# Performance work log

Measured on AMD Instinct MI355X. Metric: run time of the kernel, lower is better.

The kernel has to match this reference:

```python
import jax, jax.numpy as jnp
import numpy as np

N = 50000    # num genes (nodes)
E = 500000   # edges per edge type
T = 2        # edge types
L = 2        # gnn layers
H = 4        # attention heads
D = 64       # per-head channels (hidden // heads)
HID = 256    # hidden channels
PRE_IN = 1024
OUT = 64
EPS = 1e-5
SLOPE = 0.2  # PyG GATv2 leaky_relu negative slope


def _layer_norm(x, g, b):
    mu = x.mean(-1, keepdims=True)
    v = x.var(-1, keepdims=True)
    return (x - mu) / jnp.sqrt(v + EPS) * g + b


def _seg_softmax(score, seg, n):
    m = jax.ops.segment_max(score, seg, num_segments=n)
    ex = jnp.exp(score - m[seg])
    den = jax.ops.segment_sum(ex, seg, num_segments=n)
    return ex / (den[seg] + 1e-16)


def _gatv2_projected(x, src, dst, Wl, Wr, att, bias, Wp, bp):
    # GATv2Conv (share_weights=False, concat heads) followed by Linear projection
    n = x.shape[0]
    xl = (x @ Wl).reshape(n, H, D)
    xr = (x @ Wr).reshape(n, H, D)
    hs = xl[src]                                   # [E,H,D] messages from source
    e = jax.nn.leaky_relu(hs + xr[dst], SLOPE)     # [E,H,D]
    score = jnp.einsum('ehd,hd->eh', e, att)       # [E,H]
    alpha = _seg_softmax(score, dst, n)            # softmax over in-edges of dst
    out = jax.ops.segment_sum(hs * alpha[:, :, None], dst, num_segments=n)
    out = out.reshape(n, H * D) + bias             # concat heads + conv bias
    return out @ Wp + bp                           # ProjectedGATConv linear


def setup_inputs() -> dict:
    key = jax.random.key(0)
    ks = jax.random.split(key, 20)
    s = 0.05
    return {
        'x': jax.random.normal(ks[0], (N, PRE_IN), dtype=jnp.float32),
        'edge_index_0': jax.random.randint(ks[1], (2, E), 0, N, dtype=jnp.int32),
        'edge_index_1': jax.random.randint(ks[2], (2, E), 0, N, dtype=jnp.int32),
        'pre_W0': jax.random.normal(ks[3], (PRE_IN, HID)) * s,
        'pre_b0': jnp.zeros((HID,)),
        'pre_g0': jnp.ones((HID,)),
        'pre_be0': jnp.zeros((HID,)),
        'pre_W1': jax.random.normal(ks[4], (HID, HID)) * s,
        'pre_b1': jnp.zeros((HID,)),
        'pre_g1': jnp.ones((HID,)),
        'pre_be1': jnp.zeros((HID,)),
        # HeteroGnn: L layers x T edge types of ProjectedGATConv(GATv2)
        'gat_Wl': jax.random.normal(ks[5], (L, T, HID, H * D)) * s,
        'gat_Wr': jax.random.normal(ks[6], (L, T, HID, H * D)) * s,
        'gat_att': jax.random.normal(ks[7], (L, T, H, D)) * 0.1,
        'gat_bias': jnp.zeros((L, T, H * D)),
        'proj_W': jax.random.normal(ks[8], (L, T, H * D, HID)) * s,
        'proj_b': jnp.zeros((L, T, HID)),
        # prediction head: Linear(HID,HID) + relu + Linear(HID,OUT)
        'head_W0': jax.random.normal(ks[9], (HID, HID)) * s,
        'head_b0': jnp.zeros((HID,)),
        'head_W1': jax.random.normal(ks[10], (HID, OUT)) * s,
        'head_b1': jnp.zeros((OUT,)),
    }


def reference(x, edge_index_0, edge_index_1, pre_W0, pre_b0, pre_g0, pre_be0,
              pre_W1, pre_b1, pre_g1, pre_be1, gat_Wl, gat_Wr, gat_att,
              gat_bias, proj_W, proj_b, head_W0, head_b0, head_W1, head_b1):
    loop = jnp.arange(N, dtype=edge_index_0.dtype)  # add_self_loops=True
    edges = [(jnp.concatenate([ei[0], loop]), jnp.concatenate([ei[1], loop]))
             for ei in (edge_index_0, edge_index_1)]
    # preprocessor MLP
    h = jax.nn.relu(_layer_norm(x @ pre_W0 + pre_b0, pre_g0, pre_be0))
    h = jax.nn.relu(_layer_norm(h @ pre_W1 + pre_b1, pre_g1, pre_be1))
    # hetero GAT stack, HeteroConv aggr='sum'
    for l in range(L):
        acc = jnp.zeros((N, HID), dtype=h.dtype)
        for t in range(T):
            src, dst = edges[t]
            acc = acc + _gatv2_projected(h, src, dst, gat_Wl[l, t], gat_Wr[l, t],
                                         gat_att[l, t], gat_bias[l, t],
                                         proj_W[l, t], proj_b[l, t])
        h = jax.nn.relu(acc)
    # prediction head
    h2 = jax.nn.relu(h @ head_W0 + head_b0)
    return h2 @ head_W1 + head_b1
```

## Files before the change

kernel.cpp:

```cpp
#include <hip/hip_runtime.h>
#include <hip/hip_bf16.h>
#include <math.h>

#define N_NODES 50000
#define MP      50048
#define E_EDGES 500000
#define EPRIME  (E_EDGES + N_NODES)
#define HID     256
#define PRE_IN  1024
#define OUT_DIM 64
#define NHEAD   4
#define DHEAD   64
#define LAYERS  2
#define NTYPES  2

#define SCAN_NBLK 49
#define NPAD      (SCAN_NBLK * 1024)

typedef __attribute__((ext_vector_type(8))) short short8v;
typedef __attribute__((ext_vector_type(4))) float f32x4;
typedef _Float16 h2v __attribute__((ext_vector_type(2)));
typedef _Float16 h8v __attribute__((ext_vector_type(8)));

__device__ __forceinline__ ushort f2bf(float f) {
  uint u = __float_as_uint(f);
  u += 0x7FFF + ((u >> 16) & 1);
  return (ushort)(u >> 16);
}
__device__ __forceinline__ float bf2f(ushort u) {
  return __uint_as_float(((uint)u) << 16);
}

template<bool AF32>
__global__ __launch_bounds__(256) void gemm_k(
    const void* __restrict__ Ap,
    const ushort* __restrict__ Bt,
    int K, int M, int N,
    float*  __restrict__ Cf,
    ushort* __restrict__ Cb,
    const float* __restrict__ bias,
    const float* __restrict__ bias2,
    int do_relu, int out_f16)
{
  __shared__ ushort As[128 * 32];
  __shared__ ushort Bs[64 * 32];
  const int tid = threadIdx.x;
  const int l   = tid & 63;
  const int w   = tid >> 6;
  const int wm  = w & 1;
  const int wn  = w >> 1;
  const int bm  = blockIdx.y * 128;
  const int bn  = blockIdx.x * 64;

  f32x4 acc[4][2];
#pragma unroll
  for (int m = 0; m < 4; m++)
#pragma unroll
    for (int n = 0; n < 2; n++) acc[m][n] = (f32x4){0.f, 0.f, 0.f, 0.f};

  const int srow  = l >> 2;
  const int sslot = l & 3;

  const int brow  = tid >> 2;
  const int bslot = tid & 3;
  const int bkc   = bslot ^ ((brow >> 1) & 3);

  for (int k0 = 0; k0 < K; k0 += 32) {
    {
      const ushort* gb = Bt + (size_t)(bn + brow) * K + k0 + bkc * 8;
      __builtin_amdgcn_global_load_lds(
          (const __attribute__((address_space(1))) uint*)gb,
          (__attribute__((address_space(3))) uint*)((char*)Bs + tid * 16), 16, 0, 0);
    }
#pragma unroll
    for (int i = 0; i < 2; i++) {
      const int row = w * 32 + i * 16 + srow;
      const int kc  = sslot ^ ((row >> 1) & 3);
      const uint off = (uint)row * 64 + (uint)sslot * 16;
      if constexpr (AF32) {
        const float* ga = (const float*)Ap + (size_t)(bm + row) * K + k0 + kc * 8;
        float4 v0 = make_float4(0.f, 0.f, 0.f, 0.f);
        float4 v1 = make_float4(0.f, 0.f, 0.f, 0.f);
        if (bm + row < M) {
          v0 = *reinterpret_cast<const float4*>(ga);
          v1 = *reinterpret_cast<const float4*>(ga + 4);
        }
        short8v s;
        s[0] = (short)f2bf(v0.x); s[1] = (short)f2bf(v0.y);
        s[2] = (short)f2bf(v0.z); s[3] = (short)f2bf(v0.w);
        s[4] = (short)f2bf(v1.x); s[5] = (short)f2bf(v1.y);
        s[6] = (short)f2bf(v1.z); s[7] = (short)f2bf(v1.w);
        *reinterpret_cast<short8v*>((char*)As + off) = s;
      } else {
        const ushort* ga = (const ushort*)Ap + (size_t)(bm + row) * K + k0 + kc * 8;
        __builtin_amdgcn_global_load_lds(
            (const __attribute__((address_space(1))) uint*)ga,
            (__attribute__((address_space(3))) uint*)((char*)As + off), 16, 0, 0);
      }
    }
    __syncthreads();

    short8v a[4], b[2];
#pragma unroll
    for (int m = 0; m < 4; m++) {
      const int row = wm * 64 + m * 16 + (l & 15);
      const int kc  = (l >> 4) ^ ((row >> 1) & 3);
      a[m] = *(const short8v*)((const char*)As + row * 64 + kc * 16);
    }
#pragma unroll
    for (int n = 0; n < 2; n++) {
      const int row = wn * 32 + n * 16 + (l & 15);
      const int kc  = (l >> 4) ^ ((row >> 1) & 3);
      b[n] = *(const short8v*)((const char*)Bs + row * 64 + kc * 16);
    }
#pragma unroll
    for (int m = 0; m < 4; m++)
#pragma unroll
      for (int n = 0; n < 2; n++)
        acc[m][n] = __builtin_amdgcn_mfma_f32_16x16x32_bf16(a[m], b[n], acc[m][n], 0, 0, 0);
    __syncthreads();
  }

  const int crow0 = bm + wm * 64 + (l >> 4) * 4;
  const int ccol0 = bn + wn * 32 + (l & 15);
#pragma unroll
  for (int m = 0; m < 4; m++) {
#pragma unroll
    for (int j = 0; j < 4; j++) {
      const int grow = crow0 + m * 16 + j;
      if (grow < M) {
#pragma unroll
        for (int n = 0; n < 2; n++) {
          const int gcol = ccol0 + n * 16;
          if (gcol < N) {
            float v = acc[m][n][j];
            if (bias)  v += bias[gcol];
            if (bias2) v += bias2[gcol];
            if (do_relu) v = fmaxf(v, 0.f);
            if (Cf) Cf[(size_t)grow * N + gcol] = v;
            else if (out_f16) {
              _Float16 hv = (_Float16)v;
              Cb[(size_t)grow * N + gcol] = *(ushort*)&hv;
            } else {
              Cb[(size_t)grow * N + gcol] = f2bf(v);
            }
          }
        }
      }
    }
  }
}

__global__ void ln_relu(const float* __restrict__ in, ushort* __restrict__ out,
                        const float* __restrict__ g, const float* __restrict__ be, int n)
{
  int gid = blockIdx.x * blockDim.x + threadIdx.x;
  int row = gid >> 6;
  int lane = threadIdx.x & 63;
  if (row >= n) return;
  float4 v = *reinterpret_cast<const float4*>(in + (size_t)row * HID + lane * 4);
  float s = v.x + v.y + v.z + v.w;
  float ss = v.x * v.x + v.y * v.y + v.z * v.z + v.w * v.w;
#pragma unroll
  for (int o = 1; o < 64; o <<= 1) { s += __shfl_xor(s, o); ss += __shfl_xor(ss, o); }
  float mu = s * (1.f / 256.f);
  float var = ss * (1.f / 256.f) - mu * mu;
  float inv = rsqrtf(var + 1e-5f);
  float4 gg = *reinterpret_cast<const float4*>(g + lane * 4);
  float4 bb = *reinterpret_cast<const float4*>(be + lane * 4);
  ushort4 o4;
  o4.x = f2bf(fmaxf((v.x - mu) * inv * gg.x + bb.x, 0.f));
  o4.y = f2bf(fmaxf((v.y - mu) * inv * gg.y + bb.y, 0.f));
  o4.z = f2bf(fmaxf((v.z - mu) * inv * gg.z + bb.z, 0.f));
  o4.w = f2bf(fmaxf((v.w - mu) * inv * gg.w + bb.w, 0.f));
  *reinterpret_cast<ushort4*>(out + (size_t)row * HID + lane * 4) = o4;
}

__global__ void csr_count2(const int* __restrict__ ei0, const int* __restrict__ ei1,
                           int* __restrict__ cnt0, int* __restrict__ cnt1)
{
  int e = blockIdx.x * blockDim.x + threadIdx.x;
  if (e >= 2 * EPRIME) return;
  int type = e >= EPRIME;
  int i = type ? e - EPRIME : e;
  const int* ei = type ? ei1 : ei0;
  int* cnt = type ? cnt1 : cnt0;
  int d = (i < E_EDGES) ? ei[E_EDGES + i] : (i - E_EDGES);
  atomicAdd(&cnt[d], 1);
}

__global__ __launch_bounds__(256) void scan_p1(const int* __restrict__ cnt0,
                                               const int* __restrict__ cnt1,
                                               int* __restrict__ bsums)
{
  int type = blockIdx.x >= SCAN_NBLK;
  int blk = type ? blockIdx.x - SCAN_NBLK : blockIdx.x;
  const int* cnt = type ? cnt1 : cnt0;
  int4 v = reinterpret_cast<const int4*>(cnt)[blk * 256 + threadIdx.x];
  int s = v.x + v.y + v.z + v.w;
#pragma unroll
  for (int o = 1; o < 64; o <<= 1) s += __shfl_xor(s, o);
  __shared__ int wt[4];
  if ((threadIdx.x & 63) == 0) wt[threadIdx.x >> 6] = s;
  __syncthreads();
  if (threadIdx.x == 0) bsums[blockIdx.x] = wt[0] + wt[1] + wt[2] + wt[3];
}

__global__ void scan_p2(const int* __restrict__ bsums, int* __restrict__ boffs,
                        int* __restrict__ offs0, int* __restrict__ offs1)
{
  int t = threadIdx.x;
  if (t < 2) {
    int run = 0;
    for (int i = 0; i < SCAN_NBLK; i++) {
      boffs[t * SCAN_NBLK + i] = run;
      run += bsums[t * SCAN_NBLK + i];
    }
  }
  if (t == 2) offs0[N_NODES] = EPRIME;
  if (t == 3) offs1[N_NODES] = EPRIME;
}

__global__ __launch_bounds__(256) void scan_p3(
    const int* __restrict__ cnt0, const int* __restrict__ cnt1,
    const int* __restrict__ boffs,
    int* __restrict__ offs0, int* __restrict__ cur0,
    int* __restrict__ offs1, int* __restrict__ cur1)
{
  int type = blockIdx.x >= SCAN_NBLK;
  int blk = type ? blockIdx.x - SCAN_NBLK : blockIdx.x;
  const int* cnt = type ? cnt1 : cnt0;
  int* offs = type ? offs1 : offs0;
  int* cur  = type ? cur1 : cur0;
  const int tid = threadIdx.x, lane = tid & 63, wv = tid >> 6;
  int4 v = reinterpret_cast<const int4*>(cnt)[blk * 256 + tid];
  int e1 = v.x, e2 = e1 + v.y, e3 = e2 + v.z, T = e3 + v.w;
  int incl = T;
#pragma unroll
  for (int o = 1; o < 64; o <<= 1) {
    int nb = __shfl_up(incl, o);
    if (lane >= o) incl += nb;
  }
  __shared__ int wt[4];
  if (lane == 63) wt[wv] = incl;
  __syncthreads();
  int wexcl = 0;
  for (int i = 0; i < wv; i++) wexcl += wt[i];
  int base = boffs[blockIdx.x] + wexcl + (incl - T);
  int idx = blk * 1024 + tid * 4;
  int4 o4 = make_int4(base, base + e1, base + e2, base + e3);
  if (idx + 3 < N_NODES) {
    reinterpret_cast<int4*>(offs)[idx >> 2] = o4;
    reinterpret_cast<int4*>(cur)[idx >> 2] = o4;
  } else {
    if (idx + 0 < N_NODES) { offs[idx + 0] = o4.x; cur[idx + 0] = o4.x; }
    if (idx + 1 < N_NODES) { offs[idx + 1] = o4.y; cur[idx + 1] = o4.y; }
    if (idx + 2 < N_NODES) { offs[idx + 2] = o4.z; cur[idx + 2] = o4.z; }
    if (idx + 3 < N_NODES) { offs[idx + 3] = o4.w; cur[idx + 3] = o4.w; }
  }
}

__global__ void csr_scatter2(const int* __restrict__ ei0, const int* __restrict__ ei1,
                             int* __restrict__ cur0, int* __restrict__ cur1,
                             int* __restrict__ csr0, int* __restrict__ csr1)
{
  int e = blockIdx.x * blockDim.x + threadIdx.x;
  if (e >= 2 * EPRIME) return;
  int type = e >= EPRIME;
  int i = type ? e - EPRIME : e;
  const int* ei = type ? ei1 : ei0;
  int* cur = type ? cur1 : cur0;
  int* csr = type ? csr1 : csr0;
  int d = (i < E_EDGES) ? ei[E_EDGES + i] : (i - E_EDGES);
  int s = (i < E_EDGES) ? ei[i] : (i - E_EDGES);
  int pos = atomicAdd(&cur[d], 1);
  csr[pos] = s;
}

__global__ void csr_sort2(const int* __restrict__ offs0, int* __restrict__ csr0,
                          const int* __restrict__ offs1, int* __restrict__ csr1)
{
  int d = blockIdx.x * blockDim.x + threadIdx.x;
  if (d >= 2 * N_NODES) return;
  int type = d >= N_NODES;
  int i = type ? d - N_NODES : d;
  const int* offs = type ? offs1 : offs0;
  int* csr = type ? csr1 : csr0;
  int b = offs[i], e = offs[i + 1];
  for (int p = b + 1; p < e; p++) {
    int v = csr[p];
    int j = p - 1;
    while (j >= b && csr[j] > v) { csr[j + 1] = csr[j]; j--; }
    csr[j + 1] = v;
  }
}

#define WSEG0 262144
#define WSEG1 (WSEG0 + 65536)
#define WSEG2 (WSEG1 + 524288)
#define WSEG3 (WSEG2 + 262144)
#define WSEG4 (WSEG3 + 65536)
#define WSEG5 (WSEG4 + 32768)
__global__ void wtrans_all(const float* __restrict__ pre_W0, const float* __restrict__ pre_W1,
                           const float* __restrict__ Wl, const float* __restrict__ Wr,
                           const float* __restrict__ proj_W,
                           const float* __restrict__ head_W0, const float* __restrict__ head_W1,
                           ushort* __restrict__ W0t, ushort* __restrict__ W1t,
                           ushort* __restrict__ WcatT, ushort* __restrict__ projcatT,
                           ushort* __restrict__ hW0t, ushort* __restrict__ hW1t)
{
  int i = blockIdx.x * blockDim.x + threadIdx.x;
  if (i < WSEG0) {
    int nrow = i >> 10, k = i & 1023;
    W0t[i] = f2bf(pre_W0[(size_t)k * 256 + nrow]);
  } else if (i < WSEG1) {
    int j = i - WSEG0;
    int nrow = j >> 8, k = j & 255;
    W1t[j] = f2bf(pre_W1[(size_t)k * 256 + nrow]);
  } else if (i < WSEG2) {
    int j = i - WSEG1;
    int l = j >> 18;
    int rem = j & 262143;
    int c = rem >> 8, k = rem & 255;
    int t = c >> 9, half = (c >> 8) & 1, cc = c & 255;
    const float* W = half ? Wr : Wl;
    WcatT[j] = f2bf(W[(((size_t)l * NTYPES + t) * 256 + k) * 256 + cc]);
  } else if (i < WSEG3) {
    int j = i - WSEG2;
    int l = j >> 17;
    int rem = j & 131071;
    int n = rem >> 9, k = rem & 511;
    int t = k >> 8, kk = k & 255;
    projcatT[j] = f2bf(proj_W[(((size_t)l * NTYPES + t) * 256 + kk) * 256 + n]);
  } else if (i < WSEG4) {
    int j = i - WSEG3;
    int nrow = j >> 8, k = j & 255;
    hW0t[j] = f2bf(head_W0[(size_t)k * 256 + nrow]);
  } else if (i < WSEG5) {
    int j = i - WSEG4;
    int nrow = j >> 8, k = j & 255;
    hW1t[j] = (nrow < OUT_DIM) ? f2bf(head_W1[(size_t)k * OUT_DIM + nrow]) : (ushort)0;
  }
}

__device__ __forceinline__ float dpp8_sum(float p) {
  p += __int_as_float(__builtin_amdgcn_update_dpp(0, __float_as_int(p), 0xB1, 0xF, 0xF, true));
  p += __int_as_float(__builtin_amdgcn_update_dpp(0, __float_as_int(p), 0x4E, 0xF, 0xF, true));
  p += __int_as_float(__builtin_amdgcn_update_dpp(0, __float_as_int(p), 0x141, 0xF, 0xF, true));
  return p;
}

__device__ __forceinline__ h8v leaky8(h8v x) {
  const _Float16 c = (_Float16)0.2f;
  h8v y = x * c;
#if __has_builtin(__builtin_elementwise_max)
  return __builtin_elementwise_max(x, y);
#else
  h8v r;
#pragma unroll
  for (int i = 0; i < 8; i++) r[i] = x[i] > y[i] ? x[i] : y[i];
  return r;
#endif
}

__device__ __forceinline__ float dot8(h8v e, const h2v* a) {
  h2v e0 = {e[0], e[1]}, e1 = {e[2], e[3]}, e2 = {e[4], e[5]}, e3 = {e[6], e[7]};
#if __has_builtin(__builtin_amdgcn_fdot2)
  float s = __builtin_amdgcn_fdot2(e0, a[0], 0.f, false);
  s = __builtin_amdgcn_fdot2(e1, a[1], s, false);
  s = __builtin_amdgcn_fdot2(e2, a[2], s, false);
  s = __builtin_amdgcn_fdot2(e3, a[3], s, false);
  return s;
#else
  float s = 0.f;
#pragma unroll
  for (int i = 0; i < 8; i++) s += (float)e[i] * (float)a[i >> 1][i & 1];
  return s;
#endif
}

__global__ __launch_bounds__(256) void gat_edge3(
    const _Float16* __restrict__ xlr,
    const int* __restrict__ offs0, const int* __restrict__ csr0,
    const int* __restrict__ offs1, const int* __restrict__ csr1,
    const float* __restrict__ att,
    const float* __restrict__ bias,
    ushort* __restrict__ out, int nblk_per_type)
{
  const int type = blockIdx.x >= nblk_per_type;
  const int bid = type ? blockIdx.x - nblk_per_type : blockIdx.x;
  const int wid = (bid * 256 + threadIdx.x) >> 6;
  if (wid >= N_NODES) return;
  const int lane = threadIdx.x & 63;
  const int half = lane >> 5, li = lane & 31;
  const int* offs = type ? offs1 : offs0;
  const int* csr  = type ? csr1 : csr0;
  const int xl_col = type ? 512 : 0;

  const float* ap = att + type * 256 + li * 8;
  h2v a[4];
#pragma unroll
  for (int i = 0; i < 4; i++) {
    a[i][0] = (_Float16)ap[2 * i];
    a[i][1] = (_Float16)ap[2 * i + 1];
  }
  const h8v xr = *reinterpret_cast<const h8v*>(xlr + (size_t)wid * 1024 + xl_col + 256 + li * 8);

  const int beg = offs[wid], end = offs[wid + 1];
  const float L2E = 1.44269504f;
  float m = -1e30f, den = 0.f;
  float acc[8];
#pragma unroll
  for (int i = 0; i < 8; i++) acc[i] = 0.f;

  const int ng = (end - beg + 3) >> 2;
  for (int g = 0; g < ng; g++) {
    const int j0 = beg + 4 * g + half;
    const int j1 = j0 + 2;
    const bool v0 = j0 < end, v1 = j1 < end;
    const int s0 = csr[v0 ? j0 : beg];
    const int s1 = csr[v1 ? j1 : beg];
    const h8v hs0 = *reinterpret_cast<const h8v*>(xlr + (size_t)s0 * 1024 + xl_col + li * 8);
    const h8v hs1 = *reinterpret_cast<const h8v*>(xlr + (size_t)s1 * 1024 + xl_col + li * 8);
    float p0 = dpp8_sum(dot8(leaky8(hs0 + xr), a));
    float p1 = dpp8_sum(dot8(leaky8(hs1 + xr), a));
    if (!v0) p0 = -INFINITY;
    if (!v1) p1 = -INFINITY;
    const float pm = fmaxf(p0, p1);
    if (__any(pm > m + 4.f)) {
      const float nm = fmaxf(m, pm);
      const float so = exp2f((m - nm) * L2E);
      den *= so;
#pragma unroll
      for (int i = 0; i < 8; i++) acc[i] *= so;
      m = nm;
    }
    const float w0 = exp2f((p0 - m) * L2E);
    const float w1 = exp2f((p1 - m) * L2E);
    den += w0 + w1;
#pragma unroll
    for (int i = 0; i < 8; i++) {
      acc[i] = fmaf((float)hs0[i], w0, acc[i]);
      acc[i] = fmaf((float)hs1[i], w1, acc[i]);
    }
  }

  const float mo  = __shfl_xor(m, 32);
  const float dno = __shfl_xor(den, 32);
  const float ms = fmaxf(m, mo);
  const float fa = exp2f((m - ms) * L2E);
  const float fb = exp2f((mo - ms) * L2E);
  const float r = 1.f / (den * fa + dno * fb + 1e-16f);
  float of[8];
#pragma unroll
  for (int i = 0; i < 8; i++)
    of[i] = (acc[i] * fa + __shfl_xor(acc[i], 32) * fb) * r;

  if (half == 0) {
    const float* bp = bias + type * 256 + li * 8;
    uint4 o;
    uint pk[4];
#pragma unroll
    for (int i = 0; i < 4; i++) {
      const uint lo = f2bf(of[2 * i] + bp[2 * i]);
      const uint hi = f2bf(of[2 * i + 1] + bp[2 * i + 1]);
      pk[i] = lo | (hi << 16);
    }
    o.x = pk[0]; o.y = pk[1]; o.z = pk[2]; o.w = pk[3];
    *reinterpret_cast<uint4*>(out + (size_t)wid * 512 + type * 256 + li * 8) = o;
  }
}

extern "C" void kernel_launch(void* const* d_in, const int* in_sizes, int n_in,
                              void* d_out, int out_size, void* d_ws, size_t ws_size,
                              hipStream_t stream)
{
  const float* x        = (const float*)d_in[0];
  const int*   ei0      = (const int*)d_in[1];
  const int*   ei1      = (const int*)d_in[2];
  const float* pre_W0   = (const float*)d_in[3];
  const float* pre_b0   = (const float*)d_in[4];
  const float* pre_g0   = (const float*)d_in[5];
  const float* pre_be0  = (const float*)d_in[6];
  const float* pre_W1   = (const float*)d_in[7];
  const float* pre_b1   = (const float*)d_in[8];
  const float* pre_g1   = (const float*)d_in[9];
  const float* pre_be1  = (const float*)d_in[10];
  const float* gat_Wl   = (const float*)d_in[11];
  const float* gat_Wr   = (const float*)d_in[12];
  const float* gat_att  = (const float*)d_in[13];
  const float* gat_bias = (const float*)d_in[14];
  const float* proj_W   = (const float*)d_in[15];
  const float* proj_b   = (const float*)d_in[16];
  const float* head_W0  = (const float*)d_in[17];
  const float* head_b0  = (const float*)d_in[18];
  const float* head_W1  = (const float*)d_in[19];
  const float* head_b1  = (const float*)d_in[20];
  float* outp = (float*)d_out;

  char* ws = (char*)d_ws;
  ushort* xlr_b = (ushort*)ws; ws += (size_t)MP * 1024 * 2;
  ushort* hb    = (ushort*)ws; ws += (size_t)MP * 256 * 2;
  ushort* outt  = (ushort*)ws; ws += (size_t)MP * 512 * 2;
  float*  tmp   = (float*)outt;
  ushort* hbuf  = (ushort*)outt;
  ushort* W0t      = (ushort*)ws; ws += (size_t)256 * 1024 * 2;
  ushort* W1t      = (ushort*)ws; ws += (size_t)256 * 256 * 2;
  ushort* WcatT    = (ushort*)ws; ws += (size_t)LAYERS * 1024 * 256 * 2;
  ushort* projcatT = (ushort*)ws; ws += (size_t)LAYERS * 256 * 512 * 2;
  ushort* hW0t     = (ushort*)ws; ws += (size_t)256 * 256 * 2;
  ushort* hW1t     = (ushort*)ws; ws += (size_t)128 * 256 * 2;
  int* cnt0  = (int*)ws; ws += (size_t)NPAD * 4;
  int* cnt1  = (int*)ws; ws += (size_t)NPAD * 4;
  int* offs0 = (int*)ws; ws += (size_t)(N_NODES + 4) * 4;
  int* offs1 = (int*)ws; ws += (size_t)(N_NODES + 4) * 4;
  int* cur0  = (int*)ws; ws += (size_t)N_NODES * 4;
  int* cur1  = (int*)ws; ws += (size_t)N_NODES * 4;
  int* bsums = (int*)ws; ws += (size_t)128 * 4;
  int* boffs = (int*)ws; ws += (size_t)128 * 4;
  int* csr0  = (int*)ws; ws += (size_t)EPRIME * 4;
  int* csr1  = (int*)ws; ws += (size_t)EPRIME * 4;

  hipMemsetAsync(cnt0, 0, (size_t)2 * NPAD * 4, stream);
  const int gE2 = (2 * EPRIME + 255) / 256;
  csr_count2<<<gE2, 256, 0, stream>>>(ei0, ei1, cnt0, cnt1);
  scan_p1<<<2 * SCAN_NBLK, 256, 0, stream>>>(cnt0, cnt1, bsums);
  scan_p2<<<1, 64, 0, stream>>>(bsums, boffs, offs0, offs1);
  scan_p3<<<2 * SCAN_NBLK, 256, 0, stream>>>(cnt0, cnt1, boffs, offs0, cur0, offs1, cur1);
  csr_scatter2<<<gE2, 256, 0, stream>>>(ei0, ei1, cur0, cur1, csr0, csr1);
  csr_sort2<<<(2 * N_NODES + 255) / 256, 256, 0, stream>>>(offs0, csr0, offs1, csr1);

  wtrans_all<<<WSEG5 / 256, 256, 0, stream>>>(pre_W0, pre_W1, gat_Wl, gat_Wr, proj_W,
                                              head_W0, head_W1,
                                              W0t, W1t, WcatT, projcatT, hW0t, hW1t);

  const dim3 blk(256);
  const int gy = MP / 128;
  const int gln = (N_NODES * 64 + 255) / 256;

  gemm_k<true><<<dim3(4, gy), blk, 0, stream>>>(x, W0t, 1024, N_NODES, 256,
                                                tmp, nullptr, pre_b0, nullptr, 0, 0);
  ln_relu<<<gln, 256, 0, stream>>>(tmp, hb, pre_g0, pre_be0, N_NODES);
  gemm_k<false><<<dim3(4, gy), blk, 0, stream>>>(hb, W1t, 256, N_NODES, 256,
                                                 tmp, nullptr, pre_b1, nullptr, 0, 0);
  ln_relu<<<gln, 256, 0, stream>>>(tmp, hb, pre_g1, pre_be1, N_NODES);

  for (int l = 0; l < LAYERS; l++) {
    gemm_k<false><<<dim3(16, gy), blk, 0, stream>>>(hb, WcatT + (size_t)l * 1024 * 256,
                                                    256, N_NODES, 1024,
                                                    nullptr, xlr_b, nullptr, nullptr, 0, 1);
    gat_edge3<<<2 * gln, 256, 0, stream>>>(
        (const _Float16*)xlr_b, offs0, csr0, offs1, csr1,
        gat_att  + (size_t)l * NTYPES * NHEAD * DHEAD,
        gat_bias + (size_t)l * NTYPES * HID,
        outt, gln);
    gemm_k<false><<<dim3(4, gy), blk, 0, stream>>>(
        outt, projcatT + (size_t)l * 256 * 512, 512, N_NODES, 256,
        nullptr, hb,
        proj_b + (size_t)(l * NTYPES + 0) * HID,
        proj_b + (size_t)(l * NTYPES + 1) * HID, 1, 0);
  }

  gemm_k<false><<<dim3(4, gy), blk, 0, stream>>>(hb, hW0t, 256, N_NODES, 256,
                                                 nullptr, hbuf, head_b0, nullptr, 1, 0);
  gemm_k<false><<<dim3(1, gy), blk, 0, stream>>>(hbuf, hW1t, 256, N_NODES, OUT_DIM,
                                                 outp, nullptr, head_b1, nullptr, 0, 0);
}
```

Before: 868.9 us.

## Remap GEMM workgroups per XCD and register-prefetch next fp32 A tile

The GEMM kernel remaps its workgroup ids so consecutive tiles land on the same XCD, which is meant to improve L2 reuse of the shared A and B panels. In the fp32-A path it also loads the next k-step's A values into registers while the current step computes, hiding global load latency behind the MFMA work. This costs extra registers (16 floats per thread) and could lower occupancy. It only affects the GEMM stages, not the edge gather and scatter work.

```diff
diff --git a/kernel.cpp b/kernel.cpp
--- a/kernel.cpp
+++ b/kernel.cpp
@@ -49,8 +49,15 @@
   const int w   = tid >> 6;
   const int wm  = w & 1;
   const int wn  = w >> 1;
-  const int bm  = blockIdx.y * 128;
-  const int bn  = blockIdx.x * 64;
+
+  const int nwg  = gridDim.x * gridDim.y;
+  const int orig = blockIdx.y * gridDim.x + blockIdx.x;
+  const int qq   = nwg >> 3, rr = nwg & 7;
+  const int xcd  = orig & 7;
+  const int wgid = ((xcd < rr) ? xcd * (qq + 1) : rr * (qq + 1) + (xcd - rr) * qq)
+                   + (orig >> 3);
+  const int bm = (wgid / gridDim.x) * 128;
+  const int bn = (wgid % gridDim.x) * 64;
 
   f32x4 acc[4][2];
 #pragma unroll
@@ -64,6 +71,22 @@
   const int brow  = tid >> 2;
   const int bslot = tid & 3;
   const int bkc   = bslot ^ ((brow >> 1) & 3);
+
+  float4 pf[2][2];
+  if constexpr (AF32) {
+#pragma unroll
+    for (int i = 0; i < 2; i++) {
+      const int row = w * 32 + i * 16 + srow;
+      const int kc  = sslot ^ ((row >> 1) & 3);
+      pf[i][0] = make_float4(0.f, 0.f, 0.f, 0.f);
+      pf[i][1] = make_float4(0.f, 0.f, 0.f, 0.f);
+      if (bm + row < M) {
+        const float* ga = (const float*)Ap + (size_t)(bm + row) * K + kc * 8;
+        pf[i][0] = *reinterpret_cast<const float4*>(ga);
+        pf[i][1] = *reinterpret_cast<const float4*>(ga + 4);
+      }
+    }
+  }
 
   for (int k0 = 0; k0 < K; k0 += 32) {
     {
@@ -72,26 +95,36 @@
           (const __attribute__((address_space(1))) uint*)gb,
           (__attribute__((address_space(3))) uint*)((char*)Bs + tid * 16), 16, 0, 0);
     }
-#pragma unroll
-    for (int i = 0; i < 2; i++) {
-      const int row = w * 32 + i * 16 + srow;
-      const int kc  = sslot ^ ((row >> 1) & 3);
-      const uint off = (uint)row * 64 + (uint)sslot * 16;
-      if constexpr (AF32) {
-        const float* ga = (const float*)Ap + (size_t)(bm + row) * K + k0 + kc * 8;
-        float4 v0 = make_float4(0.f, 0.f, 0.f, 0.f);
-        float4 v1 = make_float4(0.f, 0.f, 0.f, 0.f);
-        if (bm + row < M) {
-          v0 = *reinterpret_cast<const float4*>(ga);
-          v1 = *reinterpret_cast<const float4*>(ga + 4);
+    if constexpr (AF32) {
+#pragma unroll
+      for (int i = 0; i < 2; i++) {
+        const int row = w * 32 + i * 16 + srow;
+        const uint off = (uint)row * 64 + (uint)sslot * 16;
+        short8v s;
+        s[0] = (short)f2bf(pf[i][0].x); s[1] = (short)f2bf(pf[i][0].y);
+        s[2] = (short)f2bf(pf[i][0].z); s[3] = (short)f2bf(pf[i][0].w);
+        s[4] = (short)f2bf(pf[i][1].x); s[5] = (short)f2bf(pf[i][1].y);
+        s[6] = (short)f2bf(pf[i][1].z); s[7] = (short)f2bf(pf[i][1].w);
+        *reinterpret_cast<short8v*>((char*)As + off) = s;
+      }
+      if (k0 + 32 < K) {
+#pragma unroll
+        for (int i = 0; i < 2; i++) {
+          const int row = w * 32 + i * 16 + srow;
+          const int kc  = sslot ^ ((row >> 1) & 3);
+          if (bm + row < M) {
+            const float* ga = (const float*)Ap + (size_t)(bm + row) * K + (k0 + 32) + kc * 8;
+            pf[i][0] = *reinterpret_cast<const float4*>(ga);
+            pf[i][1] = *reinterpret_cast<const float4*>(ga + 4);
+          }
         }
-        short8v s;
-        s[0] = (short)f2bf(v0.x); s[1] = (short)f2bf(v0.y);
-        s[2] = (short)f2bf(v0.z); s[3] = (short)f2bf(v0.w);
-        s[4] = (short)f2bf(v1.x); s[5] = (short)f2bf(v1.y);
-        s[6] = (short)f2bf(v1.z); s[7] = (short)f2bf(v1.w);
-        *reinterpret_cast<short8v*>((char*)As + off) = s;
-      } else {
+      }
+    } else {
+#pragma unroll
+      for (int i = 0; i < 2; i++) {
+        const int row = w * 32 + i * 16 + srow;
+        const int kc  = sslot ^ ((row >> 1) & 3);
+        const uint off = (uint)row * 64 + (uint)sslot * 16;
         const ushort* ga = (const ushort*)Ap + (size_t)(bm + row) * K + k0 + kc * 8;
         __builtin_amdgcn_global_load_lds(
             (const __attribute__((address_space(1))) uint*)ga,
```

Result: faster. 778.6 us (-10.4%).
